# Kernel optimization log

Hardware: AMD Instinct MI355X
Metric: run time of the kernel (lower is better)

Reference implementation:

```python
import jax, jax.numpy as jnp
import numpy as np

N_BRUNCH, N_RULES, N_FEA, N_BATCH = 8, 32, 16, 32768

def setup_inputs() -> dict:
    key = jax.random.key(0)
    ks = jax.random.split(key, 6)
    data = jax.random.normal(ks[0], (N_BRUNCH, N_BATCH, N_FEA), dtype=jnp.float32)
    para_mu = jax.random.normal(ks[1], (N_BRUNCH, N_RULES, N_FEA), dtype=jnp.float32)
    # sigma in [0.5, 1.5] to keep Gaussian memberships well-conditioned
    para_sigma = jax.random.uniform(ks[2], (N_BRUNCH, N_RULES, N_FEA), dtype=jnp.float32, minval=0.5, maxval=1.5)
    para_w3 = jax.random.normal(ks[3], (N_BRUNCH, N_RULES, N_FEA + 1), dtype=jnp.float32)
    w5 = jax.random.normal(ks[4], (2, N_BRUNCH), dtype=jnp.float32) * 0.1
    b5 = jax.random.normal(ks[5], (2,), dtype=jnp.float32) * 0.1
    return {"data": data, "para_mu": para_mu, "para_sigma": para_sigma, "para_w3": para_w3, "w5": w5, "b5": b5}

def reference(data, para_mu, para_sigma, para_w3, w5, b5):
    # data: [K, B, F]; params: [K, R, F] / [K, R, F+1]
    # Gaussian membership: prod_f exp(-(x-mu)^2/(2 sigma^2)) == exp(-sum_f (...))
    diff = data[:, :, None, :] - para_mu[:, None, :, :]            # [K, B, R, F]
    expo = jnp.sum(diff * diff / (2.0 * para_sigma * para_sigma)[:, None, :, :], axis=-1)  # [K, B, R]
    layer_rule = jnp.exp(-expo)                                     # [K, B, R]
    layer_norm = layer_rule / jnp.sum(layer_rule, axis=-1, keepdims=True)
    # TSK consequent: bias + w . x per (branch, rule)
    conq = para_w3[:, :, -1][:, None, :] + jnp.einsum('kbf,krf->kbr', data, para_w3[:, :, :-1])  # [K, B, R]
    tsk = jnp.sum(layer_norm * conq, axis=-1)                       # [K, B]
    logits = jnp.einsum('kb,ok->bo', tsk, w5) + b5                  # [B, 2]
    return jax.nn.softmax(logits, axis=-1)
```

## Files before the change

kernel.cpp:

```cpp
#include <hip/hip_runtime.h>

#define NK 8
#define NR 32
#define NF 16
#define NB 32768
#define LOG2E 1.4426950408889634f

typedef _Float16 f16x8  __attribute__((ext_vector_type(8)));
typedef float    f32x16 __attribute__((ext_vector_type(16)));

__global__ __launch_bounds__(512, 4) void hfnn_fused(
    const float* __restrict__ data, const float* __restrict__ mu,
    const float* __restrict__ sg,   const float* __restrict__ w3,
    const float* __restrict__ w5,   const float* __restrict__ b5,
    float* __restrict__ out)
{
    __shared__ float tl[NK][64];

    const int lane = threadIdx.x & 63;
    const int k    = threadIdx.x >> 6;
    const int h    = lane >> 5;
    const int m    = lane & 31;

    const int bbase = blockIdx.x * 64;
    float4 xv[2][2];
#pragma unroll
    for (int tau = 0; tau < 2; ++tau) {
        const float* xp = data + ((size_t)k * NB + (bbase + tau * 32 + m)) * NF + h * 8;
        xv[tau][0] = reinterpret_cast<const float4*>(xp)[0];
        xv[tau][1] = reinterpret_cast<const float4*>(xp)[1];
    }

    const float* sp = sg + ((size_t)(k * NR + m) * NF + h * 8);
    const float* mp = mu + ((size_t)(k * NR + m) * NF + h * 8);
    float4 s0 = reinterpret_cast<const float4*>(sp)[0];
    float4 s1 = reinterpret_cast<const float4*>(sp)[1];
    float4 m0 = reinterpret_cast<const float4*>(mp)[0];
    float4 m1 = reinterpret_cast<const float4*>(mp)[1];
    float sv[8] = {s0.x,s0.y,s0.z,s0.w,s1.x,s1.y,s1.z,s1.w};
    float mv[8] = {m0.x,m0.y,m0.z,m0.w,m1.x,m1.y,m1.z,m1.w};

    f16x8 frA, frB, frW;
    float cp = 0.f;
#pragma unroll
    for (int j = 0; j < 8; ++j) {
        float a = __fdividef(-(LOG2E * 0.5f), sv[j] * sv[j]);
        frA[j] = (_Float16)a;
        frB[j] = (_Float16)(-2.0f * a * mv[j]);
        cp = fmaf(a * mv[j], mv[j], cp);
    }
    float C = cp + __shfl_xor(cp, 32);

    const float* wp = w3 + (size_t)(k * NR + m) * (NF + 1) + h * 8;
#pragma unroll
    for (int j = 0; j < 8; ++j) frW[j] = (_Float16)wp[j];
    float bias = w3[(size_t)(k * NR + m) * (NF + 1) + NF];

    f32x16 c1i, c2i;
#pragma unroll
    for (int reg = 0; reg < 16; ++reg) {
        const int row = (reg & 3) + 8 * (reg >> 2) + 4 * h;
        c1i[reg] = __shfl(C, row);
        c2i[reg] = __shfl(bias, row);
    }

#pragma unroll
    for (int tau = 0; tau < 2; ++tau) {
        float4 v0 = xv[tau][0], v1 = xv[tau][1];
        f16x8 bf2, bf1;
        bf2[0] = (_Float16)v0.x; bf2[1] = (_Float16)v0.y;
        bf2[2] = (_Float16)v0.z; bf2[3] = (_Float16)v0.w;
        bf2[4] = (_Float16)v1.x; bf2[5] = (_Float16)v1.y;
        bf2[6] = (_Float16)v1.z; bf2[7] = (_Float16)v1.w;
        bf1[0] = (_Float16)(v0.x*v0.x); bf1[1] = (_Float16)(v0.y*v0.y);
        bf1[2] = (_Float16)(v0.z*v0.z); bf1[3] = (_Float16)(v0.w*v0.w);
        bf1[4] = (_Float16)(v1.x*v1.x); bf1[5] = (_Float16)(v1.y*v1.y);
        bf1[6] = (_Float16)(v1.z*v1.z); bf1[7] = (_Float16)(v1.w*v1.w);

        f32x16 s1a = __builtin_amdgcn_mfma_f32_32x32x16_f16(frA, bf1, c1i, 0, 0, 0);
        s1a        = __builtin_amdgcn_mfma_f32_32x32x16_f16(frB, bf2, s1a, 0, 0, 0);
        f32x16 s2a = __builtin_amdgcn_mfma_f32_32x32x16_f16(frW, bf2, c2i, 0, 0, 0);

        float num = 0.f, den = 0.f;
#pragma unroll
        for (int reg = 0; reg < 16; ++reg) {
            float e = __builtin_amdgcn_exp2f(s1a[reg]);
            den += e;
            num = fmaf(e, s2a[reg], num);
        }
        num += __shfl_xor(num, 32);
        den += __shfl_xor(den, 32);
        if (h == 0) tl[k][tau * 32 + m] = __fdividef(num, den);
    }
    __syncthreads();

    if (threadIdx.x < 64) {
        float l0 = b5[0], l1 = b5[1];
#pragma unroll
        for (int kk = 0; kk < NK; ++kk) {
            float t = tl[kk][lane];
            l0 = fmaf(t, w5[kk],      l0);
            l1 = fmaf(t, w5[NK + kk], l1);
        }
        float mx = fmaxf(l0, l1);
        float e0 = __expf(l0 - mx);
        float e1 = __expf(l1 - mx);
        float inv = __fdividef(1.f, e0 + e1);
        *reinterpret_cast<float2*>(out + (size_t)(blockIdx.x * 64 + lane) * 2) =
            make_float2(e0 * inv, e1 * inv);
    }
}

extern "C" void kernel_launch(void* const* d_in, const int* in_sizes, int n_in,
                              void* d_out, int out_size, void* d_ws, size_t ws_size,
                              hipStream_t stream) {
    const float* data = (const float*)d_in[0];
    const float* mu   = (const float*)d_in[1];
    const float* sg   = (const float*)d_in[2];
    const float* w3   = (const float*)d_in[3];
    const float* w5   = (const float*)d_in[4];
    const float* b5   = (const float*)d_in[5];
    float* out = (float*)d_out;

    hfnn_fused<<<NB / 64, 512, 0, stream>>>(data, mu, sg, w3, w5, b5, out);
}
```

Baseline: 9.637 us.

## Process four 32-sample tiles per block and use packed fp16 conversion and squaring

Each block now handles 128 batch columns instead of 64, which halves the grid. The per-block parameter setup (sigma/mu/w3 loads, coefficient computation, shuffles) is therefore amortized over twice as many MFMA tiles. The x and x^2 fp16 operands are now built with packed round-toward-zero conversion and packed half-precision multiplies rather than per-element fp32 squaring and conversion. Squaring in fp16 and using RTZ rounding slightly changes numerics, the larger per-thread register footprint may reduce occupancy, and the smaller grid of 256 blocks gives less parallelism to spread across CUs.

```diff
diff --git a/kernel.cpp b/kernel.cpp
--- a/kernel.cpp
+++ b/kernel.cpp
@@ -4,28 +4,40 @@
 #define NR 32
 #define NF 16
 #define NB 32768
+#define TAU 4
+#define BCOLS (32 * TAU)
 #define LOG2E 1.4426950408889634f
 
+typedef _Float16 f16x2  __attribute__((ext_vector_type(2)));
 typedef _Float16 f16x8  __attribute__((ext_vector_type(8)));
 typedef float    f32x16 __attribute__((ext_vector_type(16)));
 
-__global__ __launch_bounds__(512, 4) void hfnn_fused(
+union h8u { f16x2 h2[4]; f16x8 v; };
+
+__device__ __forceinline__ f16x2 pk_cvt(float a, float b) {
+    auto t = __builtin_amdgcn_cvt_pkrtz(a, b);
+    f16x2 r;
+    __builtin_memcpy(&r, &t, sizeof(r));
+    return r;
+}
+
+__global__ __launch_bounds__(512) void hfnn_fused(
     const float* __restrict__ data, const float* __restrict__ mu,
     const float* __restrict__ sg,   const float* __restrict__ w3,
     const float* __restrict__ w5,   const float* __restrict__ b5,
     float* __restrict__ out)
 {
-    __shared__ float tl[NK][64];
+    __shared__ float tl[NK][BCOLS];
 
     const int lane = threadIdx.x & 63;
     const int k    = threadIdx.x >> 6;
     const int h    = lane >> 5;
     const int m    = lane & 31;
 
-    const int bbase = blockIdx.x * 64;
-    float4 xv[2][2];
+    const int bbase = blockIdx.x * BCOLS;
+    float4 xv[TAU][2];
 #pragma unroll
-    for (int tau = 0; tau < 2; ++tau) {
+    for (int tau = 0; tau < TAU; ++tau) {
         const float* xp = data + ((size_t)k * NB + (bbase + tau * 32 + m)) * NF + h * 8;
         xv[tau][0] = reinterpret_cast<const float4*>(xp)[0];
         xv[tau][1] = reinterpret_cast<const float4*>(xp)[1];
@@ -65,21 +77,21 @@
     }
 
 #pragma unroll
-    for (int tau = 0; tau < 2; ++tau) {
+    for (int tau = 0; tau < TAU; ++tau) {
         float4 v0 = xv[tau][0], v1 = xv[tau][1];
-        f16x8 bf2, bf1;
-        bf2[0] = (_Float16)v0.x; bf2[1] = (_Float16)v0.y;
-        bf2[2] = (_Float16)v0.z; bf2[3] = (_Float16)v0.w;
-        bf2[4] = (_Float16)v1.x; bf2[5] = (_Float16)v1.y;
-        bf2[6] = (_Float16)v1.z; bf2[7] = (_Float16)v1.w;
-        bf1[0] = (_Float16)(v0.x*v0.x); bf1[1] = (_Float16)(v0.y*v0.y);
-        bf1[2] = (_Float16)(v0.z*v0.z); bf1[3] = (_Float16)(v0.w*v0.w);
-        bf1[4] = (_Float16)(v1.x*v1.x); bf1[5] = (_Float16)(v1.y*v1.y);
-        bf1[6] = (_Float16)(v1.z*v1.z); bf1[7] = (_Float16)(v1.w*v1.w);
+        h8u X, X2;
+        X.h2[0] = pk_cvt(v0.x, v0.y);
+        X.h2[1] = pk_cvt(v0.z, v0.w);
+        X.h2[2] = pk_cvt(v1.x, v1.y);
+        X.h2[3] = pk_cvt(v1.z, v1.w);
+        X2.h2[0] = X.h2[0] * X.h2[0];
+        X2.h2[1] = X.h2[1] * X.h2[1];
+        X2.h2[2] = X.h2[2] * X.h2[2];
+        X2.h2[3] = X.h2[3] * X.h2[3];
 
-        f32x16 s1a = __builtin_amdgcn_mfma_f32_32x32x16_f16(frA, bf1, c1i, 0, 0, 0);
-        s1a        = __builtin_amdgcn_mfma_f32_32x32x16_f16(frB, bf2, s1a, 0, 0, 0);
-        f32x16 s2a = __builtin_amdgcn_mfma_f32_32x32x16_f16(frW, bf2, c2i, 0, 0, 0);
+        f32x16 s1a = __builtin_amdgcn_mfma_f32_32x32x16_f16(frA, X2.v, c1i, 0, 0, 0);
+        s1a        = __builtin_amdgcn_mfma_f32_32x32x16_f16(frB, X.v,  s1a, 0, 0, 0);
+        f32x16 s2a = __builtin_amdgcn_mfma_f32_32x32x16_f16(frW, X.v,  c2i, 0, 0, 0);
 
         float num = 0.f, den = 0.f;
 #pragma unroll
@@ -94,11 +106,12 @@
     }
     __syncthreads();
 
-    if (threadIdx.x < 64) {
+    const int tid = threadIdx.x;
+    if (tid < BCOLS) {
         float l0 = b5[0], l1 = b5[1];
 #pragma unroll
         for (int kk = 0; kk < NK; ++kk) {
-            float t = tl[kk][lane];
+            float t = tl[kk][tid];
             l0 = fmaf(t, w5[kk],      l0);
             l1 = fmaf(t, w5[NK + kk], l1);
         }
@@ -106,7 +119,7 @@
         float e0 = __expf(l0 - mx);
         float e1 = __expf(l1 - mx);
         float inv = __fdividef(1.f, e0 + e1);
-        *reinterpret_cast<float2*>(out + (size_t)(blockIdx.x * 64 + lane) * 2) =
+        *reinterpret_cast<float2*>(out + (size_t)(bbase + tid) * 2) =
             make_float2(e0 * inv, e1 * inv);
     }
 }
@@ -122,5 +135,5 @@
     const float* b5   = (const float*)d_in[5];
     float* out = (float*)d_out;
 
-    hfnn_fused<<<NB / 64, 512, 0, stream>>>(data, mu, sg, w3, w5, b5, out);
+    hfnn_fused<<<NB / BCOLS, 512, 0, stream>>>(data, mu, sg, w3, w5, b5, out);
 }
```

After: 9.965 us. +3.4%, slower.
